# Performance work log

Hardware: AMD Instinct MI355X
Metric: run time of the kernel (lower is better)

The kernel has to match this reference:

```python
import jax, jax.numpy as jnp
import numpy as np

NUM_EXPERTS = 8
TOP_K = 2
N_EMBD = 1024
D_FFN = 2048  # 4*n_embd//top_k, already multiple of block_size=128


def setup_inputs() -> dict:
    key = jax.random.key(0)
    k1, k2, k3, k4 = jax.random.split(key, 4)
    x = jax.random.normal(k1, (4, 2048, N_EMBD), dtype=jnp.float32)
    router_w = jax.random.normal(k2, (NUM_EXPERTS, N_EMBD), dtype=jnp.float32) * 0.02
    w1 = jax.random.normal(k3, (N_EMBD, D_FFN * NUM_EXPERTS), dtype=jnp.float32) * 0.02
    w2 = jax.random.normal(k4, (D_FFN * NUM_EXPERTS, N_EMBD), dtype=jnp.float32) * 0.02
    return {"x": x, "router_w": router_w, "w1": w1, "w2": w2}


def reference(x, router_w, w1, w2):
    B, T, D = x.shape
    xf = x.reshape(B * T, D)                       # [N, d]
    N = B * T

    # Router: softmax over experts, then top-k selection and renormalization.
    logits = xf @ router_w.T                       # [N, E]
    probs = jax.nn.softmax(logits, axis=-1)
    top_v, top_i = jax.lax.top_k(probs, TOP_K)     # [N, k]
    top_v = top_v / jnp.sum(top_v, axis=-1, keepdims=True)  # norm_topk_prob=True

    # Dense [N, E] routing-weight matrix (zero for non-selected experts).
    gate = jnp.zeros((N, NUM_EXPERTS), dtype=x.dtype)
    gate = gate.at[jnp.arange(N)[:, None], top_i].set(top_v)

    w1r = w1.reshape(D, NUM_EXPERTS, D_FFN)        # expert-major column blocks
    w2r = w2.reshape(NUM_EXPERTS, D_FFN, D)

    out = jnp.zeros((N, D), dtype=x.dtype)
    for e in range(NUM_EXPERTS):
        h = jax.nn.gelu(xf @ w1r[:, e, :], approximate=False)  # [N, f]
        out = out + gate[:, e:e + 1] * (h @ w2r[e])
    return out.reshape(B, T, D)
```

## Files before the change

### kernel.cpp

```cpp
#include <hip/hip_runtime.h>
#include <hip/hip_bf16.h>
#include <cstdint>
#include <cstddef>

#define NE 8
#define N_TOK 8192
#define D_EMB 1024
#define D_FFN 2048

#define BM 128
#define BN 128
#define BK 32

typedef __attribute__((ext_vector_type(8))) short short8;
typedef __attribute__((ext_vector_type(4))) float f32x4;

__device__ __forceinline__ unsigned short f2bf(float f) {
  union { float f; unsigned int u; } c; c.f = f;
  unsigned int u = c.u;
  unsigned int r = u + 0x7FFFu + ((u >> 16) & 1u);
  return (unsigned short)(r >> 16);
}

__device__ __forceinline__ float bf2f(unsigned short u) {
  union { unsigned int u; float f; } c; c.u = ((unsigned int)u) << 16;
  return c.f;
}

__device__ __forceinline__ float gelu_f(float x) {
  float u = x * x * x * 0.044715f + x;
  float t = __expf(-1.5957691216057308f * u);
  return x * __builtin_amdgcn_rcpf(1.f + t);
}

__device__ __forceinline__ void gll16(const void* g, void* l) {
  __builtin_amdgcn_global_load_lds((const __attribute__((address_space(1))) void*)g,
                                   (__attribute__((address_space(3))) void*)l, 16, 0, 0);
}

#define SB() __builtin_amdgcn_sched_barrier(0)
#define VW(N) { asm volatile("s_waitcnt vmcnt(" #N ")" ::: "memory"); SB(); }
#define BAR() { SB(); __builtin_amdgcn_s_barrier(); SB(); }

__global__ __launch_bounds__(256) void router_k(const float* __restrict__ x,
                                                const float* __restrict__ rw,
                                                int* __restrict__ ti,
                                                float* __restrict__ tg,
                                                ushort* __restrict__ xb) {
  int w = threadIdx.x >> 6, lane = threadIdx.x & 63;
  int n = blockIdx.x * 4 + w;
  const float4* x4 = (const float4*)(x + (size_t)n * D_EMB);
  ushort4* xb4 = (ushort4*)(xb + (size_t)n * D_EMB);
  const float4* r4 = (const float4*)rw;
  float acc[NE];
#pragma unroll
  for (int e = 0; e < NE; ++e) acc[e] = 0.f;
#pragma unroll
  for (int c = 0; c < 4; ++c) {
    float4 xv = x4[c * 64 + lane];
    ushort4 o;
    o.x = f2bf(xv.x); o.y = f2bf(xv.y); o.z = f2bf(xv.z); o.w = f2bf(xv.w);
    xb4[c * 64 + lane] = o;
#pragma unroll
    for (int e = 0; e < NE; ++e) {
      float4 wv = r4[e * 256 + c * 64 + lane];
      acc[e] += xv.x * wv.x + xv.y * wv.y + xv.z * wv.z + xv.w * wv.w;
    }
  }
#pragma unroll
  for (int e = 0; e < NE; ++e) {
    float v = acc[e];
#pragma unroll
    for (int off = 32; off >= 1; off >>= 1) v += __shfl_xor(v, off);
    acc[e] = v;
  }
  if (lane == 0) {
    int e0 = 0; float v0 = acc[0];
#pragma unroll
    for (int e = 1; e < NE; ++e) if (acc[e] > v0) { v0 = acc[e]; e0 = e; }
    int e1 = -1; float v1 = -1e30f;
#pragma unroll
    for (int e = 0; e < NE; ++e) if (e != e0 && acc[e] > v1) { v1 = acc[e]; e1 = e; }
    float p1 = expf(v1 - v0);
    float g0 = 1.f / (1.f + p1);
    float g1 = p1 * g0;
    ti[2 * n] = e0; ti[2 * n + 1] = e1;
    tg[2 * n] = g0; tg[2 * n + 1] = g1;
  }
}

__global__ __launch_bounds__(256) void prep_k(const float* __restrict__ w1,
                                              const float* __restrict__ w2,
                                              const int* __restrict__ ti,
                                              ushort* __restrict__ w1t,
                                              ushort* __restrict__ w2te,
                                              int* __restrict__ counts) {
  int b = blockIdx.x;
  if (b >= 32768) {
    __shared__ int lc[NE];
    if (threadIdx.x < NE) lc[threadIdx.x] = 0;
    __syncthreads();
    int s = (b - 32768) * 512 + threadIdx.x;
    atomicAdd(&lc[ti[s]], 1);
    atomicAdd(&lc[ti[s + 256]], 1);
    __syncthreads();
    if (threadIdx.x < NE) atomicAdd(&counts[threadIdx.x], lc[threadIdx.x]);
    return;
  }
  __shared__ ushort t[32][33];
  int rl = threadIdx.x >> 3, q = threadIdx.x & 7;
  if (b < 16384) {
    int bx = b & 511, by = b >> 9;
    const int C = NE * D_FFN;
    float4 v = *(const float4*)&w1[(size_t)(by * 32 + rl) * C + bx * 32 + q * 4];
    t[rl][q * 4 + 0] = f2bf(v.x);
    t[rl][q * 4 + 1] = f2bf(v.y);
    t[rl][q * 4 + 2] = f2bf(v.z);
    t[rl][q * 4 + 3] = f2bf(v.w);
    __syncthreads();
    ushort4 o;
    o.x = t[q * 4 + 0][rl];
    o.y = t[q * 4 + 1][rl];
    o.z = t[q * 4 + 2][rl];
    o.w = t[q * 4 + 3][rl];
    *(ushort4*)&w1t[(size_t)(bx * 32 + rl) * D_EMB + by * 32 + q * 4] = o;
  } else {
    int b2 = b - 16384;
    int bx = b2 & 31, by = b2 >> 5;
    float4 v = *(const float4*)&w2[(size_t)(by * 32 + rl) * D_EMB + bx * 32 + q * 4];
    t[rl][q * 4 + 0] = f2bf(v.x);
    t[rl][q * 4 + 1] = f2bf(v.y);
    t[rl][q * 4 + 2] = f2bf(v.z);
    t[rl][q * 4 + 3] = f2bf(v.w);
    __syncthreads();
    int e = by >> 6;
    int f0 = (by & 63) * 32;
    size_t eoff = (size_t)e * (D_EMB * D_FFN);
    ushort4 o;
    o.x = t[q * 4 + 0][rl];
    o.y = t[q * 4 + 1][rl];
    o.z = t[q * 4 + 2][rl];
    o.w = t[q * 4 + 3][rl];
    *(ushort4*)&w2te[eoff + (size_t)(bx * 32 + rl) * D_FFN + f0 + q * 4] = o;
  }
}

__global__ void prefix_k(const int* __restrict__ counts, int* __restrict__ bases,
                         int* __restrict__ cursor) {
  if (threadIdx.x == 0) {
    int s = 0;
    for (int e = 0; e < NE; ++e) { bases[e] = s; cursor[e] = s; s += counts[e]; }
  }
}

__global__ __launch_bounds__(256) void scatter_k(const int* __restrict__ ti,
                                                 const float* __restrict__ tg,
                                                 int* __restrict__ cursor,
                                                 int* __restrict__ tokS,
                                                 float* __restrict__ gate) {
  __shared__ int lc[NE], lb[NE];
  if (threadIdx.x < NE) lc[threadIdx.x] = 0;
  __syncthreads();
  int s = blockIdx.x * 256 + threadIdx.x;
  int e = ti[s];
  float g = tg[s];
  int loc = atomicAdd(&lc[e], 1);
  __syncthreads();
  if (threadIdx.x < NE) lb[threadIdx.x] = atomicAdd(&cursor[threadIdx.x], lc[threadIdx.x]);
  __syncthreads();
  int pos = lb[e] + loc;
  tokS[pos] = s;
  gate[pos] = g;
}


#define STG(BUF)                                                           \
  { _Pragma("unroll") for (int j_ = 0; j_ < 2; ++j_) {                     \
      gll16(aptr[j_], &Al[BUF][ldso[j_]]);                                 \
      gll16(bptr[j_], &Bl[BUF][ldso[j_]]);                                 \
      aptr[j_] += BK; bptr[j_] += BK;                                      \
    } }

#define CMP(BUF)                                                           \
  { short8 a[4], b[4];                                                     \
    _Pragma("unroll") for (int i_ = 0; i_ < 4; ++i_)                       \
      a[i_] = *(const short8*)&Al[BUF][arow + i_ * 16 * BK];               \
    _Pragma("unroll") for (int j_ = 0; j_ < 4; ++j_)                       \
      b[j_] = *(const short8*)&Bl[BUF][brow + j_ * 16 * BK];               \
    _Pragma("unroll") for (int i_ = 0; i_ < 4; ++i_)                       \
      _Pragma("unroll") for (int j_ = 0; j_ < 4; ++j_)                     \
        acc[i_][j_] = __builtin_amdgcn_mfma_f32_16x16x32_bf16(a[i_], b[j_], acc[i_][j_], 0, 0, 0); \
  }

#define KLOOP(NT)                                                          \
  STG(0);                                                                  \
  for (int ks = 0; ks < (NT) - 2; ks += 2) {                               \
    STG(1); VW(4); BAR(); CMP(0); BAR();                                   \
    STG(0); VW(4); BAR(); CMP(1); BAR();                                   \
  }                                                                        \
  STG(1); VW(4); BAR(); CMP(0); BAR();                                     \
  VW(0); BAR(); CMP(1);

__global__ __launch_bounds__(256) void gemm1_k(const ushort* __restrict__ xb,
                                               const ushort* __restrict__ w1t,
                                               const int* __restrict__ counts,
                                               const int* __restrict__ bases,
                                               const int* __restrict__ tokS,
                                               ushort* __restrict__ h) {
  int bid = (int)blockIdx.x;
  bid = (bid & 7) * 512 + (bid >> 3);
  int e = bid >> 9;
  int rem = bid & 511;
  int mt = rem >> 4, nt = rem & 15;
  int count = counts[e];
  if (mt * BM >= count) return;
  int base = bases[e];

  __shared__ ushort Al[2][BM * BK];
  __shared__ ushort Bl[2][BN * BK];

  int tid = threadIdx.x;
  int w = tid >> 6, lane = tid & 63;

  const int ssw = (((lane & 3) ^ ((lane >> 3) & 3))) * 8;

  const ushort* aptr[2]; const ushort* bptr[2];
  int ldso[2];
#pragma unroll
  for (int j = 0; j < 2; ++j) {
    int rl = w * 32 + j * 16 + (lane >> 2);
    int pr = min(base + mt * BM + rl, base + count - 1);
    int t = tokS[pr] >> 1;
    aptr[j] = xb + (size_t)t * D_EMB + ssw;
    int c = e * D_FFN + nt * BN + rl;
    bptr[j] = w1t + (size_t)c * D_EMB + ssw;
    ldso[j] = (w * 32 + j * 16) * BK;
  }

  f32x4 zero = {0.f, 0.f, 0.f, 0.f};
  f32x4 acc[4][4];
#pragma unroll
  for (int i = 0; i < 4; ++i)
#pragma unroll
    for (int j = 0; j < 4; ++j) acc[i][j] = zero;

  int wm = w >> 1, wn = w & 1;
  const int rsw = ((lane >> 4) ^ (((lane & 15) >> 1) & 3)) * 8;
  const int arow = (wm * 64 + (lane & 15)) * BK + rsw;
  const int brow = (wn * 64 + (lane & 15)) * BK + rsw;

  KLOOP(D_EMB / BK);

  int r0 = mt * BM + wm * 64, c0 = nt * BN + wn * 64;
#pragma unroll
  for (int i = 0; i < 4; ++i) {
#pragma unroll
    for (int q = 0; q < 4; ++q) {
      int row = r0 + i * 16 + (lane >> 4) * 4 + q;
      if (row < count) {
        size_t hb = (size_t)(base + row) * D_FFN;
#pragma unroll
        for (int j = 0; j < 4; ++j) {
          h[hb + c0 + j * 16 + (lane & 15)] = f2bf(gelu_f(acc[i][j][q]));
        }
      }
    }
  }
}

__global__ __launch_bounds__(256) void gemm2_k(const ushort* __restrict__ h,
                                               const ushort* __restrict__ w2te,
                                               const int* __restrict__ counts,
                                               const int* __restrict__ bases,
                                               const int* __restrict__ tokS,
                                               const float* __restrict__ gate,
                                               ushort* __restrict__ y2) {
  int bid = (int)blockIdx.x;
  bid = (bid & 7) * 256 + (bid >> 3);
  int e = bid >> 8;
  int rem = bid & 255;
  int mt = rem >> 3, nt = rem & 7;
  int count = counts[e];
  if (mt * BM >= count) return;
  int base = bases[e];

  __shared__ ushort Al[2][BM * BK];
  __shared__ ushort Bl[2][BN * BK];

  int tid = threadIdx.x;
  int w = tid >> 6, lane = tid & 63;

  const int ssw = (((lane & 3) ^ ((lane >> 3) & 3))) * 8;

  const ushort* aptr[2]; const ushort* bptr[2];
  int ldso[2];
#pragma unroll
  for (int j = 0; j < 2; ++j) {
    int rl = w * 32 + j * 16 + (lane >> 2);
    int pr = min(base + mt * BM + rl, base + count - 1);
    aptr[j] = h + (size_t)pr * D_FFN + ssw;
    int d = nt * BN + rl;
    bptr[j] = w2te + (size_t)e * (D_EMB * D_FFN) + (size_t)d * D_FFN + ssw;
    ldso[j] = (w * 32 + j * 16) * BK;
  }

  f32x4 zero = {0.f, 0.f, 0.f, 0.f};
  f32x4 acc[4][4];
#pragma unroll
  for (int i = 0; i < 4; ++i)
#pragma unroll
    for (int j = 0; j < 4; ++j) acc[i][j] = zero;

  int wm = w >> 1, wn = w & 1;
  const int rsw = ((lane >> 4) ^ (((lane & 15) >> 1) & 3)) * 8;
  const int arow = (wm * 64 + (lane & 15)) * BK + rsw;
  const int brow = (wn * 64 + (lane & 15)) * BK + rsw;

  KLOOP(D_FFN / BK);

  int r0 = mt * BM + wm * 64, c0 = nt * BN + wn * 64;
#pragma unroll
  for (int i = 0; i < 4; ++i) {
#pragma unroll
    for (int q = 0; q < 4; ++q) {
      int row = r0 + i * 16 + (lane >> 4) * 4 + q;
      if (row < count) {
        int pr = base + row;
        float g = gate[pr];
        size_t yb = (size_t)tokS[pr] * D_EMB;
#pragma unroll
        for (int j = 0; j < 4; ++j) {
          y2[yb + c0 + j * 16 + (lane & 15)] = f2bf(g * acc[i][j][q]);
        }
      }
    }
  }
}

__global__ __launch_bounds__(256) void combine_k(const ushort* __restrict__ y2,
                                                 float* __restrict__ out) {
  int n = blockIdx.x;
  const ushort4* r0 = (const ushort4*)(y2 + (size_t)(2 * n) * D_EMB);
  const ushort4* r1 = (const ushort4*)(y2 + (size_t)(2 * n + 1) * D_EMB);
  float4* o = (float4*)(out + (size_t)n * D_EMB);
  int i = threadIdx.x;
  ushort4 a = r0[i], b = r1[i];
  float4 v;
  v.x = bf2f(a.x) + bf2f(b.x);
  v.y = bf2f(a.y) + bf2f(b.y);
  v.z = bf2f(a.z) + bf2f(b.z);
  v.w = bf2f(a.w) + bf2f(b.w);
  o[i] = v;
}

extern "C" void kernel_launch(void* const* d_in, const int* in_sizes, int n_in,
                              void* d_out, int out_size, void* d_ws, size_t ws_size,
                              hipStream_t stream) {
  const float* x  = (const float*)d_in[0];
  const float* rw = (const float*)d_in[1];
  const float* w1 = (const float*)d_in[2];
  const float* w2 = (const float*)d_in[3];
  float* out = (float*)d_out;

  char* ws = (char*)d_ws;
  size_t off = 0;
  auto alloc = [&](size_t bytes) {
    void* p = ws + off;
    off = (off + bytes + 255) & ~(size_t)255;
    return p;
  };
  int*    counts = (int*)alloc(32);
  int*    bases  = (int*)alloc(32);
  int*    cursor = (int*)alloc(32);
  int*    ti     = (int*)alloc((size_t)N_TOK * 2 * sizeof(int));
  float*  tg     = (float*)alloc((size_t)N_TOK * 2 * sizeof(float));
  int*    tokS   = (int*)alloc((size_t)N_TOK * 2 * sizeof(int));
  float*  gate   = (float*)alloc((size_t)N_TOK * 2 * sizeof(float));
  ushort* xb     = (ushort*)alloc((size_t)N_TOK * D_EMB * 2);
  ushort* w1t    = (ushort*)alloc((size_t)D_EMB * NE * D_FFN * 2);
  ushort* w2te   = (ushort*)alloc((size_t)D_EMB * NE * D_FFN * 2);
  ushort* hbuf   = (ushort*)alloc((size_t)N_TOK * 2 * D_FFN * 2);
  ushort* ybuf   = (ushort*)alloc((size_t)N_TOK * 2 * D_EMB * 2);
  (void)ws_size; (void)in_sizes; (void)n_in; (void)out_size;

  hipMemsetAsync(counts, 0, 32, stream);

  router_k<<<N_TOK / 4, 256, 0, stream>>>(x, rw, ti, tg, xb);
  prep_k<<<32800, 256, 0, stream>>>(w1, w2, ti, w1t, w2te, counts);
  prefix_k<<<1, 64, 0, stream>>>(counts, bases, cursor);
  scatter_k<<<N_TOK * 2 / 256, 256, 0, stream>>>(ti, tg, cursor, tokS, gate);
  gemm1_k<<<NE * 32 * 16, 256, 0, stream>>>(xb, w1t, counts, bases, tokS, hbuf);
  gemm2_k<<<NE * 32 * 8, 256, 0, stream>>>(hbuf, w2te, counts, bases, tokS, gate, ybuf);
  combine_k<<<N_TOK, 256, 0, stream>>>(ybuf, out);
}
```

Measured before the change: 277.2 us.

## Rewrite gemm2 as 256x256 tile, 8-wave kernel with pipelined LDS prefetch

New measurement: 303.1 us. +9.4%, slower.

```diff
diff --git a/kernel.cpp b/kernel.cpp
--- a/kernel.cpp
+++ b/kernel.cpp
@@ -41,6 +41,8 @@
 #define SB() __builtin_amdgcn_sched_barrier(0)
 #define VW(N) { asm volatile("s_waitcnt vmcnt(" #N ")" ::: "memory"); SB(); }
 #define BAR() { SB(); __builtin_amdgcn_s_barrier(); SB(); }
+#define PRI1 __builtin_amdgcn_s_setprio(1)
+#define PRI0 __builtin_amdgcn_s_setprio(0)
 
 __global__ __launch_bounds__(256) void router_k(const float* __restrict__ x,
                                                 const float* __restrict__ rw,
@@ -268,7 +270,52 @@
   }
 }
 
-__global__ __launch_bounds__(256) void gemm2_k(const ushort* __restrict__ h,
+
+#define RDA8(DST, BUF, F0)                                                 \
+  { _Pragma("unroll") for (int f_ = 0; f_ < 4; ++f_) {                     \
+      int row_ = wm * 128 + ((F0) + f_) * 16 + l15;                        \
+      DST[f_][0] = *(const short8*)&(BUF)[row_ * 64 + q0];                 \
+      DST[f_][1] = *(const short8*)&(BUF)[row_ * 64 + (q0 ^ 32)];          \
+    } }
+
+#define RDB8(DST, BUF, G0)                                                 \
+  { _Pragma("unroll") for (int g_ = 0; g_ < 2; ++g_) {                     \
+      int row_ = wn * 64 + ((G0) + g_) * 16 + l15;                         \
+      DST[g_][0] = *(const short8*)&(BUF)[row_ * 64 + q0];                 \
+      DST[g_][1] = *(const short8*)&(BUF)[row_ * 64 + (q0 ^ 32)];          \
+    } }
+
+#define QMM8(FA, FB, F0, G0)                                               \
+  { PRI1;                                                                  \
+    _Pragma("unroll") for (int f_ = 0; f_ < 4; ++f_)                       \
+    _Pragma("unroll") for (int g_ = 0; g_ < 2; ++g_)                       \
+    _Pragma("unroll") for (int k_ = 0; k_ < 2; ++k_)                       \
+      acc[(F0) + f_][(G0) + g_] = __builtin_amdgcn_mfma_f32_16x16x32_bf16( \
+          FA[f_][k_], FB[g_][k_], acc[(F0) + f_][(G0) + g_], 0, 0, 0);     \
+    PRI0; }
+
+#define GLA(J, BUF) { gll16(aP[J], (BUF) + ((J) * 64 + (tid >> 3)) * 64 + (tid & 7) * 8); aP[J] += 64; }
+#define GLB(J, BUF) { gll16(bP[J], (BUF) + ((J) * 64 + (tid >> 3)) * 64 + (tid & 7) * 8); bP[J] += 64; }
+
+#define T8(CA, CB, NA, NB, S01, S23, VN)                                   \
+  { VW(VN); BAR();                                                         \
+                                                                   \
+    if (S01) { GLA(2, NA); GLA(3, NA); }                                   \
+    RDA8(fA, CA, 0); RDB8(fB, CB, 0);                                      \
+    QMM8(fA, fB, 0, 0); BAR();                                             \
+                                                                   \
+    if (S01) { GLB(2, NB); GLB(3, NB); }                                   \
+    RDB8(fB2, CB, 2);                                                      \
+    QMM8(fA, fB2, 0, 2); BAR();                                            \
+                                                                   \
+    if (S23) { GLB(0, CB); GLB(1, CB); }                                   \
+    RDA8(fA2, CA, 4);                                                      \
+    QMM8(fA2, fB, 4, 0); BAR();                                            \
+                                                                   \
+    if (S23) { GLA(0, CA); GLA(1, CA); }                                   \
+    QMM8(fA2, fB2, 4, 2); BAR(); }
+
+__global__ __launch_bounds__(512) void gemm2_k(const ushort* __restrict__ h,
                                                const ushort* __restrict__ w2te,
                                                const int* __restrict__ counts,
                                                const int* __restrict__ bases,
@@ -276,61 +323,74 @@
                                                const float* __restrict__ gate,
                                                ushort* __restrict__ y2) {
   int bid = (int)blockIdx.x;
-  bid = (bid & 7) * 256 + (bid >> 3);
-  int e = bid >> 8;
-  int rem = bid & 255;
-  int mt = rem >> 3, nt = rem & 7;
+  bid = (bid & 7) * 64 + (bid >> 3);
+  int e = bid >> 6;
+  int rem = bid & 63;
+  int mt = rem >> 2, nt = rem & 3;
   int count = counts[e];
-  if (mt * BM >= count) return;
+  if (mt * 256 >= count) return;
   int base = bases[e];
 
-  __shared__ ushort Al[2][BM * BK];
-  __shared__ ushort Bl[2][BN * BK];
+  extern __shared__ ushort smem[];
+  ushort* Ab0 = smem;
+  ushort* Ab1 = smem + 16384;
+  ushort* Bb0 = smem + 32768;
+  ushort* Bb1 = smem + 49152;
 
   int tid = threadIdx.x;
-  int w = tid >> 6, lane = tid & 63;
-
-  const int ssw = (((lane & 3) ^ ((lane >> 3) & 3))) * 8;
-
-  const ushort* aptr[2]; const ushort* bptr[2];
-  int ldso[2];
-#pragma unroll
-  for (int j = 0; j < 2; ++j) {
-    int rl = w * 32 + j * 16 + (lane >> 2);
-    int pr = min(base + mt * BM + rl, base + count - 1);
-    aptr[j] = h + (size_t)pr * D_FFN + ssw;
-    int d = nt * BN + rl;
-    bptr[j] = w2te + (size_t)e * (D_EMB * D_FFN) + (size_t)d * D_FFN + ssw;
-    ldso[j] = (w * 32 + j * 16) * BK;
+  int wv = tid >> 6, lane = tid & 63;
+  int wm = wv >> 2, wn = wv & 3;
+  const int l15 = lane & 15;
+  const int q0 = ((lane >> 4) ^ (lane & 7)) * 8;
+  const int swc = (((tid & 7) ^ ((tid >> 3) & 7))) * 8;
+
+  const ushort* aP[4]; const ushort* bP[4];
+#pragma unroll
+  for (int r = 0; r < 4; ++r) {
+    int R = r * 64 + (tid >> 3);
+    int pr = min(base + mt * 256 + R, base + count - 1);
+    aP[r] = h + (size_t)pr * D_FFN + swc;
+    int d = nt * 256 + R;
+    bP[r] = w2te + (size_t)e * (D_EMB * D_FFN) + (size_t)d * D_FFN + swc;
   }
 
   f32x4 zero = {0.f, 0.f, 0.f, 0.f};
-  f32x4 acc[4][4];
-#pragma unroll
-  for (int i = 0; i < 4; ++i)
+  f32x4 acc[8][4];
+#pragma unroll
+  for (int i = 0; i < 8; ++i)
 #pragma unroll
     for (int j = 0; j < 4; ++j) acc[i][j] = zero;
 
-  int wm = w >> 1, wn = w & 1;
-  const int rsw = ((lane >> 4) ^ (((lane & 15) >> 1) & 3)) * 8;
-  const int arow = (wm * 64 + (lane & 15)) * BK + rsw;
-  const int brow = (wn * 64 + (lane & 15)) * BK + rsw;
-
-  KLOOP(D_FFN / BK);
-
-  int r0 = mt * BM + wm * 64, c0 = nt * BN + wn * 64;
-#pragma unroll
-  for (int i = 0; i < 4; ++i) {
+  short8 fA[4][2], fA2[4][2], fB[2][2], fB2[2][2];
+
+  GLB(0, Bb0); GLB(1, Bb0);
+  GLA(0, Ab0); GLA(1, Ab0);
+  GLA(2, Ab0); GLA(3, Ab0);
+  GLB(2, Bb0); GLB(3, Bb0);
+  GLB(0, Bb1); GLB(1, Bb1);
+  GLA(0, Ab1); GLA(1, Ab1);
+
+  const int NT = D_FFN / 64;
+  for (int t = 0; t < NT - 2; t += 2) {
+    T8(Ab0, Bb0, Ab1, Bb1, 1, 1, 4);
+    T8(Ab1, Bb1, Ab0, Bb0, 1, 1, 4);
+  }
+  T8(Ab0, Bb0, Ab1, Bb1, 1, 0, 4);
+  T8(Ab1, Bb1, Ab0, Bb0, 0, 0, 0);
+
+  int r0 = mt * 256 + wm * 128, c0 = nt * 256 + wn * 64;
+#pragma unroll
+  for (int f = 0; f < 8; ++f) {
 #pragma unroll
     for (int q = 0; q < 4; ++q) {
-      int row = r0 + i * 16 + (lane >> 4) * 4 + q;
+      int row = r0 + f * 16 + (lane >> 4) * 4 + q;
       if (row < count) {
         int pr = base + row;
         float g = gate[pr];
         size_t yb = (size_t)tokS[pr] * D_EMB;
 #pragma unroll
-        for (int j = 0; j < 4; ++j) {
-          y2[yb + c0 + j * 16 + (lane & 15)] = f2bf(g * acc[i][j][q]);
+        for (int g_ = 0; g_ < 4; ++g_) {
+          y2[yb + c0 + g_ * 16 + l15] = f2bf(g * acc[f][g_][q]);
         }
       }
     }
@@ -383,6 +443,8 @@
   ushort* ybuf   = (ushort*)alloc((size_t)N_TOK * 2 * D_EMB * 2);
   (void)ws_size; (void)in_sizes; (void)n_in; (void)out_size;
 
+  hipFuncSetAttribute((const void*)gemm2_k, hipFuncAttributeMaxDynamicSharedMemorySize, 131072);
+
   hipMemsetAsync(counts, 0, 32, stream);
 
   router_k<<<N_TOK / 4, 256, 0, stream>>>(x, rw, ti, tg, xb);
@@ -390,6 +452,6 @@
   prefix_k<<<1, 64, 0, stream>>>(counts, bases, cursor);
   scatter_k<<<N_TOK * 2 / 256, 256, 0, stream>>>(ti, tg, cursor, tokS, gate);
   gemm1_k<<<NE * 32 * 16, 256, 0, stream>>>(xb, w1t, counts, bases, tokS, hbuf);
-  gemm2_k<<<NE * 32 * 8, 256, 0, stream>>>(hbuf, w2te, counts, bases, tokS, gate, ybuf);
+  gemm2_k<<<NE * 16 * 4, 512, 131072, stream>>>(hbuf, w2te, counts, bases, tokS, gate, ybuf);
   combine_k<<<N_TOK, 256, 0, stream>>>(ybuf, out);
 }
```
